# Performance work log

Measured on AMD Instinct MI355X. Metric: run time of the kernel, lower is better.

Reference implementation:

```python
import jax, jax.numpy as jnp
import numpy as np

N_NODES = 50000
BN_EPS = 1e-5


def sage_conv(x, src, dst, Wl, Wr, b):
    # mean-aggregate neighbor features: message from src -> dst
    msg = x[src]                                             # [E, Din]
    s = jax.ops.segment_sum(msg, dst, num_segments=N_NODES)  # [N, Din]
    cnt = jax.ops.segment_sum(jnp.ones((src.shape[0],), x.dtype), dst,
                              num_segments=N_NODES)          # [N]
    mean = s / jnp.maximum(cnt, 1.0)[:, None]
    # PyG SAGEConv: lin_l(aggregated) (+bias) + lin_r(self), root_weight=True
    return mean @ Wl + b + x @ Wr


def batch_norm(x, gamma, beta):
    mu = jnp.mean(x, axis=0)
    var = jnp.var(x, axis=0)
    return (x - mu) * jax.lax.rsqrt(var + BN_EPS) * gamma + beta


def setup_inputs() -> dict:
    key = jax.random.key(0)
    ks = jax.random.split(key, 16)
    D_IN, D_H, D_OUT = 128, 128, 64
    x = jax.random.normal(ks[0], (N_NODES, D_IN), dtype=jnp.float32)
    edge_index = jax.random.randint(ks[1], (2, 800000), 0, N_NODES, dtype=jnp.int32)

    def xavier(k, din, dout):
        lim = float(np.sqrt(6.0 / (din + dout)))
        return jax.random.uniform(k, (din, dout), jnp.float32, -lim, lim)

    return {
        "x": x, "edge_index": edge_index,
        "Wl0": xavier(ks[2], D_IN, D_H), "Wr0": xavier(ks[3], D_IN, D_H),
        "b0": jnp.zeros((D_H,), jnp.float32),
        "g0": jnp.ones((D_H,), jnp.float32), "be0": jnp.zeros((D_H,), jnp.float32),
        "Wl1": xavier(ks[4], D_H, D_H), "Wr1": xavier(ks[5], D_H, D_H),
        "b1": jnp.zeros((D_H,), jnp.float32),
        "g1": jnp.ones((D_H,), jnp.float32), "be1": jnp.zeros((D_H,), jnp.float32),
        "Wl2": xavier(ks[6], D_H, D_OUT), "Wr2": xavier(ks[7], D_H, D_OUT),
        "b2": jnp.zeros((D_OUT,), jnp.float32),
    }


def reference(x, edge_index, Wl0, Wr0, b0, g0, be0,
              Wl1, Wr1, b1, g1, be1, Wl2, Wr2, b2):
    src, dst = edge_index[0], edge_index[1]
    h = sage_conv(x, src, dst, Wl0, Wr0, b0)
    h = jax.nn.relu(batch_norm(h, g0, be0))
    h = sage_conv(h, src, dst, Wl1, Wr1, b1)
    h = jax.nn.relu(batch_norm(h, g1, be1))
    h = sage_conv(h, src, dst, Wl2, Wr2, b2)
    return jax.nn.log_softmax(h, axis=-1)
```

## Files before the change

### kernel.cpp

```cpp
#include <hip/hip_runtime.h>
#include <hip/hip_bf16.h>

#define D_IN 128
#define D_OUT 64
#define BN_EPS 1e-5f
#define NB_PART 512

typedef short short8 __attribute__((ext_vector_type(8)));
typedef float f32x4 __attribute__((ext_vector_type(4)));
typedef float f32x2 __attribute__((ext_vector_type(2)));
typedef unsigned short ushort_t;
typedef unsigned int uint_t;

__device__ __forceinline__ float bf16lo(uint_t v) { return __uint_as_float(v << 16); }
__device__ __forceinline__ float bf16hi(uint_t v) { return __uint_as_float(v & 0xffff0000u); }
__device__ __forceinline__ ushort_t f2bf(float f) {
    union { __hip_bfloat16 h; ushort_t u; } cv;
    cv.h = __float2bfloat16(f);
    return cv.u;
}
__device__ __forceinline__ f32x4 ntload4(const float* p) {
    return __builtin_nontemporal_load((const f32x4*)p);
}


__global__ void hist_kernel(const int* __restrict__ dst, int* __restrict__ cnt, int E) {
    int i = blockIdx.x * 256 + threadIdx.x;
    if (i < E) atomicAdd(&cnt[__builtin_nontemporal_load(&dst[i])], 1);
}

__global__ void scan_part_kernel(const int* __restrict__ cnt, int* __restrict__ bsum, int n) {
    int i = blockIdx.x * 256 + threadIdx.x;
    int v = (i < n) ? cnt[i] : 0;
#pragma unroll
    for (int off = 1; off < 64; off <<= 1) v += __shfl_xor(v, off);
    __shared__ int ws[4];
    int lane = threadIdx.x & 63, wid = threadIdx.x >> 6;
    if (lane == 0) ws[wid] = v;
    __syncthreads();
    if (threadIdx.x == 0) bsum[blockIdx.x] = ws[0] + ws[1] + ws[2] + ws[3];
}

__global__ void scan_mid_kernel(const int* __restrict__ bsum, int* __restrict__ bpre,
                                int* __restrict__ offs, int PB, int n) {
    int t = threadIdx.x;
    int v = (t < PB) ? bsum[t] : 0;
    int lane = t & 63, wid = t >> 6;
    int sc = v;
#pragma unroll
    for (int off = 1; off < 64; off <<= 1) {
        int u = __shfl_up(sc, off);
        if (lane >= off) sc += u;
    }
    __shared__ int ws[4];
    if (lane == 63) ws[wid] = sc;
    __syncthreads();
    int wb = 0;
    for (int w = 0; w < 4; w++) if (w < wid) wb += ws[w];
    int incl = sc + wb;
    if (t < PB) bpre[t] = incl - v;
    if (t == PB - 1) offs[n] = incl;
}

__global__ void scan_final_kernel(const int* __restrict__ cnt, const int* __restrict__ bpre,
                                  int* __restrict__ offs, int n) {
    int b = blockIdx.x, t = threadIdx.x;
    int i = b * 256 + t;
    int v = (i < n) ? cnt[i] : 0;
    int lane = t & 63, wid = t >> 6;
    int sc = v;
#pragma unroll
    for (int off = 1; off < 64; off <<= 1) {
        int u = __shfl_up(sc, off);
        if (lane >= off) sc += u;
    }
    __shared__ int ws[4];
    if (lane == 63) ws[wid] = sc;
    __syncthreads();
    int wb = 0;
    for (int w = 0; w < 4; w++) if (w < wid) wb += ws[w];
    if (i < n) offs[i] = bpre[b] + wb + sc - v;
}

__global__ void scatter_kernel(const int* __restrict__ src, const int* __restrict__ dst,
                               int* __restrict__ cursor, ushort_t* __restrict__ sorted_src,
                               int E, int passW) {
    int lo = blockIdx.y * passW, hi = lo + passW;
    int i = blockIdx.x * 256 + threadIdx.x;
    if (i < E) {
        int d = __builtin_nontemporal_load(&dst[i]);
        if (d >= lo && d < hi) {
            int s = __builtin_nontemporal_load(&src[i]);
            int p = atomicAdd(&cursor[d], 1);
            sorted_src[p] = (ushort_t)s;
        }
    }
}


__global__ void wswz_kernel(const float* __restrict__ Wl0, const float* __restrict__ Wr0,
                            const float* __restrict__ Wl1, const float* __restrict__ Wr1,
                            const float* __restrict__ Wl2, const float* __restrict__ Wr2,
                            short* __restrict__ o0l, short* __restrict__ o0r,
                            short* __restrict__ o1l, short* __restrict__ o1r,
                            short* __restrict__ o2l, short* __restrict__ o2r) {
    int layer = blockIdx.z;
    int Nn = (layer == 2) ? 64 : 128;
    const float* W;
    short* out;
    if (layer == 0) { W = blockIdx.y ? Wr0 : Wl0; out = blockIdx.y ? o0r : o0l; }
    else if (layer == 1) { W = blockIdx.y ? Wr1 : Wl1; out = blockIdx.y ? o1r : o1l; }
    else { W = blockIdx.y ? Wr2 : Wl2; out = blockIdx.y ? o2r : o2l; }
    int g = blockIdx.x * 256 + threadIdx.x;
    int nchunks = (Nn / 16) * 4;
    int chunk = g >> 6, lane = g & 63;
    if (chunk >= nchunks) return;
    int nf = chunk >> 2, kk = chunk & 3;
    short8 s;
#pragma unroll
    for (int j = 0; j < 8; j++) {
        float v = W[(size_t)(kk * 32 + (lane >> 4) * 8 + j) * Nn + nf * 16 + (lane & 15)];
        s[j] = (short)f2bf(v);
    }
    *(short8*)&out[((size_t)(chunk << 6) + lane) * 8] = s;
}


template <int TN, bool BN>
__global__ __launch_bounds__(TN == 128 ? 256 : 128)
void gemm2_mfma(const float* __restrict__ A, const short* __restrict__ WlF,
                const short* __restrict__ WrF, ushort_t* __restrict__ Yb,
                float* __restrict__ Z, const float* __restrict__ stats,
                const float* __restrict__ gamma, const float* __restrict__ beta, int M) {
    __shared__ short As[64 * 136];
    __shared__ float sc[128], sh[128];
    const int tid = threadIdx.x;
    const int lane = tid & 63;
    const int w = tid >> 6;
    const int row0 = blockIdx.x * 64;
    const int NT = (TN == 128) ? 256 : 128;

    if (BN) {
        if (tid < 128) {
            float invM = 1.0f / (float)M;
            float mu = stats[tid] * invM;
            float var = stats[128 + tid] * invM - mu * mu;
            float scale = gamma[tid] * rsqrtf(var + BN_EPS);
            sc[tid] = scale;
            sh[tid] = beta[tid] - mu * scale;
        }
        __syncthreads();
    }

    for (int c = tid; c < 1024; c += NT) {
        int r = c >> 4, off = (c & 15) * 8;
        short8 v8 = {0, 0, 0, 0, 0, 0, 0, 0};
        if (row0 + r < M) {
            const float* ap = &A[(size_t)(row0 + r) * 128 + off];
            f32x4 f0 = ntload4(ap);
            f32x4 f1 = ntload4(ap + 4);
            if (BN) {
#pragma unroll
                for (int j = 0; j < 4; j++) {
                    f0[j] = fmaxf(f0[j] * sc[off + j] + sh[off + j], 0.f);
                    f1[j] = fmaxf(f1[j] * sc[off + 4 + j] + sh[off + 4 + j], 0.f);
                }
            }
#pragma unroll
            for (int j = 0; j < 4; j++) {
                v8[j] = (short)f2bf(f0[j]);
                v8[4 + j] = (short)f2bf(f1[j]);
            }
        }
        *(short8*)&As[r * 136 + off] = v8;
    }
    __syncthreads();

    const short* WF;
    bool isY;
    int col0;
    if (TN == 128) {
        isY = (w < 2);
        WF = isY ? WlF : WrF;
        col0 = (w & 1) * 64;
    } else {
        isY = (w == 0);
        WF = isY ? WlF : WrF;
        col0 = 0;
    }

    short8 a[4][4];
#pragma unroll
    for (int m = 0; m < 4; m++)
#pragma unroll
        for (int kk = 0; kk < 4; kk++)
            a[m][kk] = *(const short8*)&As[(m * 16 + (lane & 15)) * 136 + kk * 32 + (lane >> 4) * 8];

    f32x4 acc[4][4];
#pragma unroll
    for (int m = 0; m < 4; m++)
#pragma unroll
        for (int n = 0; n < 4; n++) acc[m][n] = (f32x4){0.f, 0.f, 0.f, 0.f};

#pragma unroll
    for (int kk = 0; kk < 4; kk++) {
#pragma unroll
        for (int n = 0; n < 4; n++) {
            short8 b = *(const short8*)&WF[(size_t)(((col0 >> 4) + n) * 4 + kk) * 512 + lane * 8];
#pragma unroll
            for (int m = 0; m < 4; m++)
                acc[m][n] = __builtin_amdgcn_mfma_f32_16x16x32_bf16(a[m][kk], b, acc[m][n], 0, 0, 0);
        }
    }

#pragma unroll
    for (int m = 0; m < 4; m++) {
#pragma unroll
        for (int i = 0; i < 4; i++) {
            int gr = row0 + m * 16 + (lane >> 4) * 4 + i;
            if (gr < M) {
                if (isY) {
#pragma unroll
                    for (int n = 0; n < 4; n++)
                        Yb[(size_t)gr * TN + col0 + n * 16 + (lane & 15)] = f2bf(acc[m][n][i]);
                } else {
#pragma unroll
                    for (int n = 0; n < 4; n++)
                        Z[(size_t)gr * TN + col0 + n * 16 + (lane & 15)] = acc[m][n][i];
                }
            }
        }
    }
}


__global__ __launch_bounds__(256) void agg128_kernel(const ushort_t* __restrict__ Yb,
                                                     const int* __restrict__ offs,
                                                     const ushort_t* __restrict__ sorted_src,
                                                     const float* __restrict__ bias,
                                                     float* __restrict__ H, int N) {
    int node = blockIdx.x * 4 + (threadIdx.x >> 6);
    int lane = threadIdx.x & 63;
    if (node >= N) return;
    int s0 = offs[node], s1 = offs[node + 1];
    float a0 = 0.f, a1 = 0.f;
    int k = s0;
    for (; k + 4 <= s1; k += 4) {
        int i0 = __builtin_nontemporal_load(&sorted_src[k]);
        int i1 = __builtin_nontemporal_load(&sorted_src[k + 1]);
        int i2 = __builtin_nontemporal_load(&sorted_src[k + 2]);
        int i3 = __builtin_nontemporal_load(&sorted_src[k + 3]);
        uint_t v0 = *(const uint_t*)&Yb[(size_t)i0 * 128 + lane * 2];
        uint_t v1 = *(const uint_t*)&Yb[(size_t)i1 * 128 + lane * 2];
        uint_t v2 = *(const uint_t*)&Yb[(size_t)i2 * 128 + lane * 2];
        uint_t v3 = *(const uint_t*)&Yb[(size_t)i3 * 128 + lane * 2];
        a0 += bf16lo(v0) + bf16lo(v1) + bf16lo(v2) + bf16lo(v3);
        a1 += bf16hi(v0) + bf16hi(v1) + bf16hi(v2) + bf16hi(v3);
    }
    for (; k < s1; k++) {
        uint_t v = *(const uint_t*)&Yb[(size_t)sorted_src[k] * 128 + lane * 2];
        a0 += bf16lo(v);
        a1 += bf16hi(v);
    }
    float inv = 1.0f / fmaxf((float)(s1 - s0), 1.0f);
    float2 b = *(const float2*)&bias[lane * 2];
    f32x2* hp = (f32x2*)&H[(size_t)node * 128 + lane * 2];
    f32x2 h = __builtin_nontemporal_load(hp);
    h[0] += a0 * inv + b.x;
    h[1] += a1 * inv + b.y;
    __builtin_nontemporal_store(h, hp);
}


__global__ __launch_bounds__(256) void agg_lsm_kernel(const ushort_t* __restrict__ Yb,
                                                      const int* __restrict__ offs,
                                                      const ushort_t* __restrict__ sorted_src,
                                                      const float* __restrict__ bias,
                                                      const float* __restrict__ Z,
                                                      float* __restrict__ out, int N) {
    int node = blockIdx.x * 4 + (threadIdx.x >> 6);
    int lane = threadIdx.x & 63;
    int half = lane >> 5, l = lane & 31;
    if (node >= N) return;
    int s0 = offs[node], s1 = offs[node + 1];
    float a0 = 0.f, a1 = 0.f;
    for (int k = s0 + half; k < s1; k += 2) {
        uint_t v = *(const uint_t*)&Yb[(size_t)__builtin_nontemporal_load(&sorted_src[k]) * 64 + l * 2];
        a0 += bf16lo(v);
        a1 += bf16hi(v);
    }
    a0 += __shfl_xor(a0, 32);
    a1 += __shfl_xor(a1, 32);
    float inv = 1.0f / fmaxf((float)(s1 - s0), 1.0f);
    f32x2 zb = __builtin_nontemporal_load((const f32x2*)&Z[(size_t)node * 64 + l * 2]);
    float2 bb = *(const float2*)&bias[l * 2];
    float v0 = zb[0] + a0 * inv + bb.x;
    float v1 = zb[1] + a1 * inv + bb.y;
    float m = fmaxf(v0, v1);
#pragma unroll
    for (int off = 16; off; off >>= 1) m = fmaxf(m, __shfl_xor(m, off));
    float s = expf(v0 - m) + expf(v1 - m);
#pragma unroll
    for (int off = 16; off; off >>= 1) s += __shfl_xor(s, off);
    float ls = logf(s);
    if (half == 0) {
        f32x2 o;
        o[0] = v0 - m - ls;
        o[1] = v1 - m - ls;
        __builtin_nontemporal_store(o, (f32x2*)&out[(size_t)node * 64 + l * 2]);
    }
}


__global__ __launch_bounds__(256) void bn_part_kernel(const float* __restrict__ H,
                                                      float* __restrict__ P, int M) {
    int b = blockIdx.x;
    int R = (M + NB_PART - 1) / NB_PART;
    int r0 = b * R, r1 = min(r0 + R, M);
    int colg = (threadIdx.x & 31) * 4;
    int rowoff = threadIdx.x >> 5;
    f32x4 s = {0.f, 0.f, 0.f, 0.f}, s2 = {0.f, 0.f, 0.f, 0.f};
    for (int r = r0 + rowoff; r < r1; r += 8) {
        f32x4 v = ntload4(&H[(size_t)r * 128 + colg]);
        s += v;
        s2 += v * v;
    }
    __shared__ float ls[256][8];
#pragma unroll
    for (int j = 0; j < 4; j++) {
        ls[threadIdx.x][j] = s[j];
        ls[threadIdx.x][4 + j] = s2[j];
    }
    __syncthreads();
    if (threadIdx.x < 32) {
#pragma unroll
        for (int j = 0; j < 8; j++) {
            float a = 0.f;
#pragma unroll
            for (int k = 0; k < 8; k++) a += ls[threadIdx.x + 32 * k][j];
            if (j < 4) P[(size_t)b * 256 + threadIdx.x * 4 + j] = a;
            else P[(size_t)b * 256 + 128 + threadIdx.x * 4 + (j - 4)] = a;
        }
    }
}

__global__ __launch_bounds__(1024) void bn_reduce_kernel(const float* __restrict__ P,
                                                         float* __restrict__ stats) {
    int c = threadIdx.x & 255, q = threadIdx.x >> 8;
    float acc = 0.f;
    for (int i = q * (NB_PART / 4); i < (q + 1) * (NB_PART / 4); i++)
        acc += P[(size_t)i * 256 + c];
    __shared__ float ls[4][256];
    ls[q][c] = acc;
    __syncthreads();
    if (threadIdx.x < 256) stats[c] = ls[0][c] + ls[1][c] + ls[2][c] + ls[3][c];
}


extern "C" void kernel_launch(void* const* d_in, const int* in_sizes, int n_in,
                              void* d_out, int out_size, void* d_ws, size_t ws_size,
                              hipStream_t stream) {
    const float* x   = (const float*)d_in[0];
    const int*   ei  = (const int*)d_in[1];
    const float* Wl0 = (const float*)d_in[2];
    const float* Wr0 = (const float*)d_in[3];
    const float* b0  = (const float*)d_in[4];
    const float* g0  = (const float*)d_in[5];
    const float* be0 = (const float*)d_in[6];
    const float* Wl1 = (const float*)d_in[7];
    const float* Wr1 = (const float*)d_in[8];
    const float* b1  = (const float*)d_in[9];
    const float* g1  = (const float*)d_in[10];
    const float* be1 = (const float*)d_in[11];
    const float* Wl2 = (const float*)d_in[12];
    const float* Wr2 = (const float*)d_in[13];
    const float* b2  = (const float*)d_in[14];

    const int N = in_sizes[0] / D_IN;
    const int E = in_sizes[1] / 2;
    const int PB = (N + 255) / 256;

    float* H = (float*)d_ws;
    float* Z2 = H + (size_t)N * D_IN;
    ushort_t* Yb = (ushort_t*)(Z2 + (size_t)N * D_OUT);
    int* cnt    = (int*)(Yb + (size_t)N * D_IN);
    int* offs   = cnt + N;
    int* cursor = offs + N + 1;
    int* bsum   = cursor + N;
    int* bpre   = bsum + 256;
    ushort_t* sorted = (ushort_t*)(bpre + 256);
    float* stats = (float*)(sorted + E + (E & 1));
    float* P = stats + 512;
    short* WlF0 = (short*)(P + NB_PART * 256);
    short* WrF0 = WlF0 + 16384;
    short* WlF1 = WrF0 + 16384;
    short* WrF1 = WlF1 + 16384;
    short* WlF2 = WrF1 + 16384;
    short* WrF2 = WlF2 + 8192;

    const int eb = (E + 255) / 256;

    hipMemsetAsync(cnt, 0, (size_t)N * sizeof(int), stream);
    hist_kernel<<<eb, 256, 0, stream>>>(ei + E, cnt, E);
    scan_part_kernel<<<PB, 256, 0, stream>>>(cnt, bsum, N);
    scan_mid_kernel<<<1, 256, 0, stream>>>(bsum, bpre, offs, PB, N);
    scan_final_kernel<<<PB, 256, 0, stream>>>(cnt, bpre, offs, N);
    hipMemcpyAsync(cursor, offs, (size_t)N * sizeof(int), hipMemcpyDeviceToDevice, stream);
    scatter_kernel<<<dim3(eb, 2), 256, 0, stream>>>(ei, ei + E, cursor, sorted, E, (N + 1) / 2);

    wswz_kernel<<<dim3(8, 2, 3), 256, 0, stream>>>(Wl0, Wr0, Wl1, Wr1, Wl2, Wr2,
                                                   WlF0, WrF0, WlF1, WrF1, WlF2, WrF2);

    const int gb = (N + 63) / 64;
    const int ab = (N + 3) / 4;

    gemm2_mfma<128, false><<<gb, 256, 0, stream>>>(x, WlF0, WrF0, Yb, H,
                                                   nullptr, nullptr, nullptr, N);
    agg128_kernel<<<ab, 256, 0, stream>>>(Yb, offs, sorted, b0, H, N);
    bn_part_kernel<<<NB_PART, 256, 0, stream>>>(H, P, N);
    bn_reduce_kernel<<<1, 1024, 0, stream>>>(P, stats);

    gemm2_mfma<128, true><<<gb, 256, 0, stream>>>(H, WlF1, WrF1, Yb, H,
                                                  stats, g0, be0, N);
    agg128_kernel<<<ab, 256, 0, stream>>>(Yb, offs, sorted, b1, H, N);
    bn_part_kernel<<<NB_PART, 256, 0, stream>>>(H, P, N);
    bn_reduce_kernel<<<1, 1024, 0, stream>>>(P, stats + 256);

    gemm2_mfma<64, true><<<gb, 128, 0, stream>>>(H, WlF2, WrF2, Yb, Z2,
                                                 stats + 256, g1, be1, N);
    agg_lsm_kernel<<<ab, 256, 0, stream>>>(Yb, offs, sorted, b2, Z2, (float*)d_out, N);
}
```

Measured before the change: 415.5 us.

## Widen gather unroll, pack two nodes per wave in final aggregation, drop cursor memcpy

The scan writes the cursor array directly, so the separate device-to-device copy is no longer needed. The 128-wide aggregation loop now issues eight gathers in flight instead of four. The final log-softmax aggregation maps two nodes per wavefront, one per half-wave, instead of splitting one node's edges across halves, which halves the launched blocks and removes the cross-half shuffle. The BN reduce loop is also unrolled. The aim is more memory-level parallelism and less launch and copy overhead, at the cost of more registers and more divergence between half-waves of unequal degree.

Result: faster. 372.8 us (-10.3%).

```diff
diff --git a/kernel.cpp b/kernel.cpp
--- a/kernel.cpp
+++ b/kernel.cpp
@@ -63,7 +63,7 @@
 }
 
 __global__ void scan_final_kernel(const int* __restrict__ cnt, const int* __restrict__ bpre,
-                                  int* __restrict__ offs, int n) {
+                                  int* __restrict__ offs, int* __restrict__ cursor, int n) {
     int b = blockIdx.x, t = threadIdx.x;
     int i = b * 256 + t;
     int v = (i < n) ? cnt[i] : 0;
@@ -79,7 +79,11 @@
     __syncthreads();
     int wb = 0;
     for (int w = 0; w < 4; w++) if (w < wid) wb += ws[w];
-    if (i < n) offs[i] = bpre[b] + wb + sc - v;
+    if (i < n) {
+        int e = bpre[b] + wb + sc - v;
+        offs[i] = e;
+        cursor[i] = e;
+    }
 }
 
 __global__ void scatter_kernel(const int* __restrict__ src, const int* __restrict__ dst,
@@ -245,17 +249,30 @@
     int s0 = offs[node], s1 = offs[node + 1];
     float a0 = 0.f, a1 = 0.f;
     int k = s0;
-    for (; k + 4 <= s1; k += 4) {
-        int i0 = __builtin_nontemporal_load(&sorted_src[k]);
-        int i1 = __builtin_nontemporal_load(&sorted_src[k + 1]);
-        int i2 = __builtin_nontemporal_load(&sorted_src[k + 2]);
-        int i3 = __builtin_nontemporal_load(&sorted_src[k + 3]);
-        uint_t v0 = *(const uint_t*)&Yb[(size_t)i0 * 128 + lane * 2];
-        uint_t v1 = *(const uint_t*)&Yb[(size_t)i1 * 128 + lane * 2];
-        uint_t v2 = *(const uint_t*)&Yb[(size_t)i2 * 128 + lane * 2];
-        uint_t v3 = *(const uint_t*)&Yb[(size_t)i3 * 128 + lane * 2];
-        a0 += bf16lo(v0) + bf16lo(v1) + bf16lo(v2) + bf16lo(v3);
-        a1 += bf16hi(v0) + bf16hi(v1) + bf16hi(v2) + bf16hi(v3);
+    for (; k + 8 <= s1; k += 8) {
+        int idx[8];
+#pragma unroll
+        for (int j = 0; j < 8; j++) idx[j] = __builtin_nontemporal_load(&sorted_src[k + j]);
+        uint_t v[8];
+#pragma unroll
+        for (int j = 0; j < 8; j++) v[j] = *(const uint_t*)&Yb[(size_t)idx[j] * 128 + lane * 2];
+#pragma unroll
+        for (int j = 0; j < 8; j++) {
+            a0 += bf16lo(v[j]);
+            a1 += bf16hi(v[j]);
+        }
+    }
+    if (k + 4 <= s1) {
+        int idx[4];
+#pragma unroll
+        for (int j = 0; j < 4; j++) idx[j] = __builtin_nontemporal_load(&sorted_src[k + j]);
+#pragma unroll
+        for (int j = 0; j < 4; j++) {
+            uint_t v = *(const uint_t*)&Yb[(size_t)idx[j] * 128 + lane * 2];
+            a0 += bf16lo(v);
+            a1 += bf16hi(v);
+        }
+        k += 4;
     }
     for (; k < s1; k++) {
         uint_t v = *(const uint_t*)&Yb[(size_t)sorted_src[k] * 128 + lane * 2];
@@ -278,19 +295,30 @@
                                                       const float* __restrict__ bias,
                                                       const float* __restrict__ Z,
                                                       float* __restrict__ out, int N) {
-    int node = blockIdx.x * 4 + (threadIdx.x >> 6);
+    int wv = blockIdx.x * 4 + (threadIdx.x >> 6);
     int lane = threadIdx.x & 63;
     int half = lane >> 5, l = lane & 31;
+    int node = wv * 2 + half;
     if (node >= N) return;
     int s0 = offs[node], s1 = offs[node + 1];
     float a0 = 0.f, a1 = 0.f;
-    for (int k = s0 + half; k < s1; k += 2) {
-        uint_t v = *(const uint_t*)&Yb[(size_t)__builtin_nontemporal_load(&sorted_src[k]) * 64 + l * 2];
+    int k = s0;
+    for (; k + 4 <= s1; k += 4) {
+        int idx[4];
+#pragma unroll
+        for (int j = 0; j < 4; j++) idx[j] = __builtin_nontemporal_load(&sorted_src[k + j]);
+#pragma unroll
+        for (int j = 0; j < 4; j++) {
+            uint_t v = *(const uint_t*)&Yb[(size_t)idx[j] * 64 + l * 2];
+            a0 += bf16lo(v);
+            a1 += bf16hi(v);
+        }
+    }
+    for (; k < s1; k++) {
+        uint_t v = *(const uint_t*)&Yb[(size_t)sorted_src[k] * 64 + l * 2];
         a0 += bf16lo(v);
         a1 += bf16hi(v);
     }
-    a0 += __shfl_xor(a0, 32);
-    a1 += __shfl_xor(a1, 32);
     float inv = 1.0f / fmaxf((float)(s1 - s0), 1.0f);
     f32x2 zb = __builtin_nontemporal_load((const f32x2*)&Z[(size_t)node * 64 + l * 2]);
     float2 bb = *(const float2*)&bias[l * 2];
@@ -303,12 +331,10 @@
 #pragma unroll
     for (int off = 16; off; off >>= 1) s += __shfl_xor(s, off);
     float ls = logf(s);
-    if (half == 0) {
-        f32x2 o;
-        o[0] = v0 - m - ls;
-        o[1] = v1 - m - ls;
-        __builtin_nontemporal_store(o, (f32x2*)&out[(size_t)node * 64 + l * 2]);
-    }
+    f32x2 o;
+    o[0] = v0 - m - ls;
+    o[1] = v1 - m - ls;
+    __builtin_nontemporal_store(o, (f32x2*)&out[(size_t)node * 64 + l * 2]);
 }
 
 
@@ -348,6 +374,7 @@
                                                          float* __restrict__ stats) {
     int c = threadIdx.x & 255, q = threadIdx.x >> 8;
     float acc = 0.f;
+#pragma unroll 8
     for (int i = q * (NB_PART / 4); i < (q + 1) * (NB_PART / 4); i++)
         acc += P[(size_t)i * 256 + c];
     __shared__ float ls[4][256];
@@ -404,8 +431,7 @@
     hist_kernel<<<eb, 256, 0, stream>>>(ei + E, cnt, E);
     scan_part_kernel<<<PB, 256, 0, stream>>>(cnt, bsum, N);
     scan_mid_kernel<<<1, 256, 0, stream>>>(bsum, bpre, offs, PB, N);
-    scan_final_kernel<<<PB, 256, 0, stream>>>(cnt, bpre, offs, N);
-    hipMemcpyAsync(cursor, offs, (size_t)N * sizeof(int), hipMemcpyDeviceToDevice, stream);
+    scan_final_kernel<<<PB, 256, 0, stream>>>(cnt, bpre, offs, cursor, N);
     scatter_kernel<<<dim3(eb, 2), 256, 0, stream>>>(ei, ei + E, cursor, sorted, E, (N + 1) / 2);
 
     wswz_kernel<<<dim3(8, 2, 3), 256, 0, stream>>>(Wl0, Wr0, Wl1, Wr1, Wl2, Wr2,
@@ -413,6 +439,7 @@
 
     const int gb = (N + 63) / 64;
     const int ab = (N + 3) / 4;
+    const int ab2 = (N + 7) / 8;
 
     gemm2_mfma<128, false><<<gb, 256, 0, stream>>>(x, WlF0, WrF0, Yb, H,
                                                    nullptr, nullptr, nullptr, N);
@@ -428,5 +455,5 @@
 
     gemm2_mfma<64, true><<<gb, 128, 0, stream>>>(H, WlF2, WrF2, Yb, Z2,
                                                  stats + 256, g1, be1, N);
-    agg_lsm_kernel<<<ab, 256, 0, stream>>>(Yb, offs, sorted, b2, Z2, (float*)d_out, N);
-}
+    agg_lsm_kernel<<<ab2, 256, 0, stream>>>(Yb, offs, sorted, b2, Z2, (float*)d_out, N);
+}
```
